# Kernel tuning notes

Measured on AMD Instinct MI355X. Metric: run time of the kernel, lower is better.

## Reference

```python
import jax, jax.numpy as jnp
import numpy as np

# SO(2)-equivariant linear (eSCN, arXiv:2302.03655), 'uv' fully-connected mode.
# Irreps l = 0..4 on both input and output sides.
LS = (0, 1, 2, 3, 4)
N, C_IN, C_OUT = 8192, 128, 128


def _build_paths():
    """Enumerate sparse-product entries (in_idx, out_idx, weight_idx, coef).

    Per (l_in, l_out) path: one weight for m=0, and for each 1<=m<=min(l_in,l_out)
    a (w_re, w_im) pair acting as the 2x2 rotation
        y_{+m} = w_re x_{+m} - w_im x_{-m}
        y_{-m} = w_im x_{+m} + w_re x_{-m}
    path_norm scales every path into an output irrep by 1/sqrt(#paths).
    """
    dims = [2 * l + 1 for l in LS]
    off = np.concatenate([[0], np.cumsum(dims)[:-1]])  # start of each irrep block
    pn = 1.0 / np.sqrt(len(LS))  # every output irrep receives len(LS) paths
    in_idx, out_idx, w_idx, coef = [], [], [], []
    w = 0
    for lo_i, lo in enumerate(LS):
        for li_i, li in enumerate(LS):
            oi, oo = int(off[li_i]), int(off[lo_i])
            # m = 0 component (index l within a (2l+1) block)
            in_idx.append(oi + li); out_idx.append(oo + lo); w_idx.append(w); coef.append(pn)
            w += 1
            for m in range(1, min(li, lo) + 1):
                ip, im = oi + li + m, oi + li - m   # input +m / -m positions
                op, om = oo + lo + m, oo + lo - m   # output +m / -m positions
                w_re, w_im = w, w + 1
                w += 2
                for ii, jj, ww, s in ((ip, op, w_re, 1.0), (im, om, w_re, 1.0),
                                      (ip, om, w_im, 1.0), (im, op, w_im, -1.0)):
                    in_idx.append(ii); out_idx.append(jj); w_idx.append(ww); coef.append(s * pn)
    return (np.asarray(in_idx), np.asarray(out_idx), np.asarray(w_idx),
            np.asarray(coef, np.float32), w, int(sum(dims)))


IN_IDX, OUT_IDX, W_IDX, COEF, NUM_W, DIM = _build_paths()  # NUM_W=85, DIM=25, T=145


def setup_inputs() -> dict:
    key = jax.random.key(0)
    k1, k2 = jax.random.split(key)
    x = jax.random.normal(k1, (N, DIM, C_IN), jnp.float32)
    wgt = jax.random.normal(k2, (NUM_W, C_IN, C_OUT), jnp.float32) * (C_IN ** -0.5)
    return {"input": x, "weight": wgt}


def reference(input, weight):
    coef = jnp.asarray(COEF)
    # gather one row per sparse-product entry: [N, T, C_in]
    x = input[:, IN_IDX, :] * coef[None, :, None]
    # per-entry vec-mat with the entry's weight matrix: [N, T, C_out]
    y = jnp.einsum('ntc,tcd->ntd', x, weight[W_IDX])
    # scatter-add entries into their output irrep components
    out = jnp.zeros((input.shape[0], DIM, weight.shape[-1]), y.dtype)
    return out.at[:, OUT_IDX, :].add(y)
```

## Files before the change

kernel.cpp:

```cpp
#include <hip/hip_runtime.h>
#include <cstdint>
#include <cstddef>

#define NROWS 8192
#define DIM   25
#define CIN   128
#define COUT  128
#define MAXT  160

struct Tables {
  int   w_idx[MAXT];
  float coef[MAXT];
  int   o_start[DIM + 1];
  int   e_in[MAXT];
  int   e_t[MAXT];
  int   o_lpt[DIM];
  int   T;
};

constexpr Tables build_tables() {
  Tables tb{};
  int off[5] = {0, 1, 4, 9, 16};
  const float pn = 0.44721359549995793f;
  int in_idx[MAXT] = {}, out_idx[MAXT] = {}, widx[MAXT] = {};
  float cf[MAXT] = {};
  int T = 0, w = 0;
  for (int lo = 0; lo < 5; ++lo) {
    for (int li = 0; li < 5; ++li) {
      int oi = off[li], oo = off[lo];
      in_idx[T] = oi + li; out_idx[T] = oo + lo; widx[T] = w; cf[T] = pn; ++T; ++w;
      int mm = li < lo ? li : lo;
      for (int m = 1; m <= mm; ++m) {
        int ip = oi + li + m, im = oi + li - m;
        int op = oo + lo + m, om = oo + lo - m;
        int wre = w, wim = w + 1; w += 2;
        in_idx[T] = ip; out_idx[T] = op; widx[T] = wre; cf[T] = pn;  ++T;
        in_idx[T] = im; out_idx[T] = om; widx[T] = wre; cf[T] = pn;  ++T;
        in_idx[T] = ip; out_idx[T] = om; widx[T] = wim; cf[T] = pn;  ++T;
        in_idx[T] = im; out_idx[T] = op; widx[T] = wim; cf[T] = -pn; ++T;
      }
    }
  }
  tb.T = T;
  for (int t = 0; t < T; ++t) { tb.w_idx[t] = widx[t]; tb.coef[t] = cf[t]; }
  int pos = 0;
  for (int o = 0; o < DIM; ++o) {
    tb.o_start[o] = pos;
    for (int t = 0; t < T; ++t)
      if (out_idx[t] == o) { tb.e_in[pos] = in_idx[t]; tb.e_t[pos] = t; ++pos; }
  }
  tb.o_start[DIM] = pos;
  for (int i = 0; i < DIM; ++i) tb.o_lpt[i] = i;
  for (int i = 0; i < DIM; ++i) {
    int best = i;
    for (int j = i + 1; j < DIM; ++j) {
      int nb = tb.o_start[tb.o_lpt[best] + 1] - tb.o_start[tb.o_lpt[best]];
      int nj = tb.o_start[tb.o_lpt[j] + 1] - tb.o_start[tb.o_lpt[j]];
      if (nj > nb) best = j;
    }
    int tmp = tb.o_lpt[i]; tb.o_lpt[i] = tb.o_lpt[best]; tb.o_lpt[best] = tmp;
  }
  return tb;
}

__constant__ Tables TAB = build_tables();

__device__ __forceinline__ uint16_t f2bf(float f) {
  uint32_t u = __float_as_uint(f);
  uint32_t r = (u + 0x7FFFu + ((u >> 16) & 1u)) >> 16;
  return (uint16_t)r;
}

__device__ __forceinline__ void load_lds16(const void* g, void* l) {
  __builtin_amdgcn_global_load_lds(
      (const __attribute__((address_space(1))) uint32_t*)g,
      (__attribute__((address_space(3))) uint32_t*)l, 16, 0, 0);
}

typedef __bf16 v8bf __attribute__((ext_vector_type(8)));
typedef float  v4f  __attribute__((ext_vector_type(4)));

#define NCVT (NROWS * DIM * CIN / 4 / 512)
#define NWB  (145 * 4)

__global__ void prep_kernel(const float* __restrict__ X, uint16_t* __restrict__ Y,
                            const float* __restrict__ W, uint16_t* __restrict__ Bt) {
  if (blockIdx.x < NCVT) {
    int i0 = blockIdx.x * 512 + threadIdx.x;
    #pragma unroll
    for (int r = 0; r < 2; ++r) {
      int i = i0 + (r << 8);
      float4 v = ((const float4*)X)[i];
      ushort4 o;
      o.x = f2bf(v.x); o.y = f2bf(v.y); o.z = f2bf(v.z); o.w = f2bf(v.w);
      ((ushort4*)Y)[i] = o;
    }
  } else {
    __shared__ float tile[128][33];
    int b  = blockIdx.x - NCVT;
    int t  = b >> 2;
    int d0 = (b & 3) << 5;
    int w  = TAB.w_idx[t];
    float cf = TAB.coef[t];
    const float* Wp = W + (size_t)w * CIN * COUT;
    uint16_t* Bp = Bt + (size_t)t * CIN * COUT;
    int tid = threadIdx.x;
    {
      int dcol = tid & 31, cbase = tid >> 5;
      #pragma unroll
      for (int r = 0; r < 16; ++r) {
        int c = (r << 3) + cbase;
        tile[c][dcol] = cf * Wp[(size_t)c * COUT + d0 + dcol];
      }
    }
    __syncthreads();
    {
      int c = tid & 127, dbase = tid >> 7;
      #pragma unroll
      for (int r = 0; r < 16; ++r) {
        int dd = (r << 1) + dbase;
        Bp[(size_t)(d0 + dd) * CIN + c] = f2bf(tile[c][dd]);
      }
    }
  }
}

__global__ __launch_bounds__(512) void so2_gemm(
    const uint16_t* __restrict__ Xb,
    const uint16_t* __restrict__ Bt,
    float* __restrict__ Out) {
  __shared__ __align__(16) uint16_t As[256 * 64];
  __shared__ __align__(16) uint16_t Bs[128 * 64];

  const int lb   = blockIdx.x;
  const int xcd  = lb & 7;
  const int slot = lb >> 3;
  const int o    = TAB.o_lpt[slot % 25];
  const int nt   = xcd + ((slot / 25) << 3);
  const int n0   = nt << 8;

  const int e0 = TAB.o_start[o];
  const int nE = TAB.o_start[o + 1] - e0;

  const int tid  = threadIdx.x;
  const int w    = tid >> 6;
  const int l    = tid & 63;

  const int srow = (w << 3) + (l >> 3);
  const int slt  = l & 7;
  const int ssrc = ((slt ^ (l >> 3)) << 3);

  const int lr   = l & 15;
  const int quad = l >> 4;
  const int wr   = (w & 3) << 6;
  const int wc   = (w >> 2) << 6;

  v4f acc[4][4];
  #pragma unroll
  for (int i = 0; i < 4; ++i)
    #pragma unroll
    for (int j = 0; j < 4; ++j)
      acc[i][j] = v4f{0.f, 0.f, 0.f, 0.f};

  const int nIter = nE << 1;
  for (int ki = 0; ki < nIter; ++ki) {
    const int e    = e0 + (ki >> 1);
    const int kk   = (ki & 1) << 6;
    const int irow = TAB.e_in[e];
    const int trow = TAB.e_t[e];

    const uint16_t* gA = Xb + ((size_t)(n0 + srow) * DIM + irow) * CIN + kk + ssrc;
    const uint16_t* gB = Bt + ((size_t)trow * COUT + srow) * CIN + kk + ssrc;

    if (ki) __syncthreads();
    #pragma unroll
    for (int j = 0; j < 4; ++j) {
      const int m = (j << 6) + srow;
      load_lds16(gA + (size_t)(j << 6) * (DIM * CIN), &As[m * 64 + slt * 8]);
    }
    #pragma unroll
    for (int j = 0; j < 2; ++j) {
      const int m = (j << 6) + srow;
      load_lds16(gB + (size_t)(j << 6) * CIN, &Bs[m * 64 + slt * 8]);
    }
    __syncthreads();

    #pragma unroll
    for (int kk2 = 0; kk2 < 2; ++kk2) {
      const int s = (((kk2 << 2) + quad) ^ (lr & 7)) << 3;
      v8bf a[4], b[4];
      #pragma unroll
      for (int i = 0; i < 4; ++i) {
        a[i] = *(const v8bf*)(&As[(wr + (i << 4) + lr) * 64 + s]);
        b[i] = *(const v8bf*)(&Bs[(wc + (i << 4) + lr) * 64 + s]);
      }
      #pragma unroll
      for (int i = 0; i < 4; ++i)
        #pragma unroll
        for (int j = 0; j < 4; ++j)
          acc[i][j] = __builtin_amdgcn_mfma_f32_16x16x32_bf16(a[i], b[j],
                                                              acc[i][j], 0, 0, 0);
    }
  }

  #pragma unroll
  for (int i = 0; i < 4; ++i) {
    #pragma unroll
    for (int r = 0; r < 4; ++r) {
      const int n = n0 + wr + (i << 4) + (quad << 2) + r;
      float* op = Out + ((size_t)n * DIM + o) * COUT + wc + lr;
      #pragma unroll
      for (int j = 0; j < 4; ++j)
        op[j << 4] = acc[i][j][r];
    }
  }
}

extern "C" void kernel_launch(void* const* d_in, const int* in_sizes, int n_in,
                              void* d_out, int out_size, void* d_ws, size_t ws_size,
                              hipStream_t stream) {
  const float* X = (const float*)d_in[0];
  const float* W = (const float*)d_in[1];
  float* Out = (float*)d_out;

  uint16_t* Xb = (uint16_t*)d_ws;
  uint16_t* Bt = (uint16_t*)((char*)d_ws + (size_t)NROWS * DIM * CIN * 2);

  prep_kernel<<<NCVT + NWB, 256, 0, stream>>>(X, Xb, W, Bt);
  so2_gemm<<<DIM * (NROWS / 256), 512, 0, stream>>>(Xb, Bt, Out);
}
```

Measured before the change: 232.5 us.

## Fuse fp32-to-bf16 input conversion into GEMM A-tile loads

Drops the separate pass that converts the whole input to bf16 in workspace. The GEMM now streams fp32 input rows into LDS with an adjusted XOR swizzle and converts to bf16 in registers before each MFMA. This removes a full read-write pass over the input, but doubles the A-tile LDS footprint (64 KB fp32) and the global bytes fetched per A tile, which may lower occupancy. Each input row is also re-read in fp32 by many output-irrep blocks.

```diff
diff --git a/kernel.cpp b/kernel.cpp
--- a/kernel.cpp
+++ b/kernel.cpp
@@ -80,56 +80,49 @@
 typedef __bf16 v8bf __attribute__((ext_vector_type(8)));
 typedef float  v4f  __attribute__((ext_vector_type(4)));
 
-#define NCVT (NROWS * DIM * CIN / 4 / 512)
+__device__ __forceinline__ v8bf cvt8(float4 p, float4 q) {
+  v8bf v;
+  v[0] = (__bf16)p.x; v[1] = (__bf16)p.y; v[2] = (__bf16)p.z; v[3] = (__bf16)p.w;
+  v[4] = (__bf16)q.x; v[5] = (__bf16)q.y; v[6] = (__bf16)q.z; v[7] = (__bf16)q.w;
+  return v;
+}
+
 #define NWB  (145 * 4)
 
-__global__ void prep_kernel(const float* __restrict__ X, uint16_t* __restrict__ Y,
-                            const float* __restrict__ W, uint16_t* __restrict__ Bt) {
-  if (blockIdx.x < NCVT) {
-    int i0 = blockIdx.x * 512 + threadIdx.x;
-    #pragma unroll
-    for (int r = 0; r < 2; ++r) {
-      int i = i0 + (r << 8);
-      float4 v = ((const float4*)X)[i];
-      ushort4 o;
-      o.x = f2bf(v.x); o.y = f2bf(v.y); o.z = f2bf(v.z); o.w = f2bf(v.w);
-      ((ushort4*)Y)[i] = o;
-    }
-  } else {
-    __shared__ float tile[128][33];
-    int b  = blockIdx.x - NCVT;
-    int t  = b >> 2;
-    int d0 = (b & 3) << 5;
-    int w  = TAB.w_idx[t];
-    float cf = TAB.coef[t];
-    const float* Wp = W + (size_t)w * CIN * COUT;
-    uint16_t* Bp = Bt + (size_t)t * CIN * COUT;
-    int tid = threadIdx.x;
-    {
-      int dcol = tid & 31, cbase = tid >> 5;
-      #pragma unroll
-      for (int r = 0; r < 16; ++r) {
-        int c = (r << 3) + cbase;
-        tile[c][dcol] = cf * Wp[(size_t)c * COUT + d0 + dcol];
-      }
-    }
-    __syncthreads();
-    {
-      int c = tid & 127, dbase = tid >> 7;
-      #pragma unroll
-      for (int r = 0; r < 16; ++r) {
-        int dd = (r << 1) + dbase;
-        Bp[(size_t)(d0 + dd) * CIN + c] = f2bf(tile[c][dd]);
-      }
+__global__ void prep_kernel(const float* __restrict__ W, uint16_t* __restrict__ Bt) {
+  __shared__ float tile[128][33];
+  int b  = blockIdx.x;
+  int t  = b >> 2;
+  int d0 = (b & 3) << 5;
+  int w  = TAB.w_idx[t];
+  float cf = TAB.coef[t];
+  const float* Wp = W + (size_t)w * CIN * COUT;
+  uint16_t* Bp = Bt + (size_t)t * CIN * COUT;
+  int tid = threadIdx.x;
+  {
+    int dcol = tid & 31, cbase = tid >> 5;
+    #pragma unroll
+    for (int r = 0; r < 16; ++r) {
+      int c = (r << 3) + cbase;
+      tile[c][dcol] = cf * Wp[(size_t)c * COUT + d0 + dcol];
+    }
+  }
+  __syncthreads();
+  {
+    int c = tid & 127, dbase = tid >> 7;
+    #pragma unroll
+    for (int r = 0; r < 16; ++r) {
+      int dd = (r << 1) + dbase;
+      Bp[(size_t)(d0 + dd) * CIN + c] = f2bf(tile[c][dd]);
     }
   }
 }
 
 __global__ __launch_bounds__(512) void so2_gemm(
-    const uint16_t* __restrict__ Xb,
+    const float* __restrict__ X,
     const uint16_t* __restrict__ Bt,
     float* __restrict__ Out) {
-  __shared__ __align__(16) uint16_t As[256 * 64];
+  __shared__ __align__(16) float    Asf[256 * 64];
   __shared__ __align__(16) uint16_t Bs[128 * 64];
 
   const int lb   = blockIdx.x;
@@ -146,6 +139,12 @@
   const int w    = tid >> 6;
   const int l    = tid & 63;
 
+  const int arow4 = (w << 2) + (l >> 4);
+  const int achk  = l & 15;
+  const int asrc  = ((achk ^ (arow4 & 7)) << 2);
+  const float* gAr = X + (size_t)(n0 + arow4) * (DIM * CIN) + asrc;
+  float* lAr = &Asf[(size_t)arow4 * 64 + achk * 4];
+
   const int srow = (w << 3) + (l >> 3);
   const int slt  = l & 7;
   const int ssrc = ((slt ^ (l >> 3)) << 3);
@@ -154,6 +153,7 @@
   const int quad = l >> 4;
   const int wr   = (w & 3) << 6;
   const int wc   = (w >> 2) << 6;
+  const int ar   = lr & 7;
 
   v4f acc[4][4];
   #pragma unroll
@@ -169,15 +169,13 @@
     const int irow = TAB.e_in[e];
     const int trow = TAB.e_t[e];
 
-    const uint16_t* gA = Xb + ((size_t)(n0 + srow) * DIM + irow) * CIN + kk + ssrc;
+    const float*    gA = gAr + (size_t)irow * CIN + kk;
     const uint16_t* gB = Bt + ((size_t)trow * COUT + srow) * CIN + kk + ssrc;
 
     if (ki) __syncthreads();
     #pragma unroll
-    for (int j = 0; j < 4; ++j) {
-      const int m = (j << 6) + srow;
-      load_lds16(gA + (size_t)(j << 6) * (DIM * CIN), &As[m * 64 + slt * 8]);
-    }
+    for (int j = 0; j < 8; ++j)
+      load_lds16(gA + (size_t)(j << 5) * (DIM * CIN), lAr + (j << 5) * 64);
     #pragma unroll
     for (int j = 0; j < 2; ++j) {
       const int m = (j << 6) + srow;
@@ -187,12 +185,16 @@
 
     #pragma unroll
     for (int kk2 = 0; kk2 < 2; ++kk2) {
-      const int s = (((kk2 << 2) + quad) ^ (lr & 7)) << 3;
+      const int s8 = (kk2 << 2) + quad;
+      const int sb = (s8 ^ (lr & 7)) << 3;
       v8bf a[4], b[4];
       #pragma unroll
       for (int i = 0; i < 4; ++i) {
-        a[i] = *(const v8bf*)(&As[(wr + (i << 4) + lr) * 64 + s]);
-        b[i] = *(const v8bf*)(&Bs[(wc + (i << 4) + lr) * 64 + s]);
+        const float* pa = &Asf[(wr + (i << 4) + lr) * 64];
+        float4 f0 = *(const float4*)(pa + ((((s8 << 1))     ^ ar) << 2));
+        float4 f1 = *(const float4*)(pa + ((((s8 << 1) | 1) ^ ar) << 2));
+        a[i] = cvt8(f0, f1);
+        b[i] = *(const v8bf*)(&Bs[(wc + (i << 4) + lr) * 64 + sb]);
       }
       #pragma unroll
       for (int i = 0; i < 4; ++i)
@@ -223,9 +225,8 @@
   const float* W = (const float*)d_in[1];
   float* Out = (float*)d_out;
 
-  uint16_t* Xb = (uint16_t*)d_ws;
-  uint16_t* Bt = (uint16_t*)((char*)d_ws + (size_t)NROWS * DIM * CIN * 2);
-
-  prep_kernel<<<NCVT + NWB, 256, 0, stream>>>(X, Xb, W, Bt);
-  so2_gemm<<<DIM * (NROWS / 256), 512, 0, stream>>>(Xb, Bt, Out);
-}
+  uint16_t* Bt = (uint16_t*)d_ws;
+
+  prep_kernel<<<NWB, 256, 0, stream>>>(W, Bt);
+  so2_gemm<<<DIM * (NROWS / 256), 512, 0, stream>>>(X, Bt, Out);
+}
```

After: 263.1 us. +13.2%, slower.
